# Kernel tuning notes

Hardware: AMD Instinct MI355X
Metric: run time of the kernel (lower is better)

The kernel has to match this reference:

```python
import jax, jax.numpy as jnp
import numpy as np
import math

INPUT_SIZE = 512
DK = 64
B, N = 8, 2048

def setup_inputs() -> dict:
    key = jax.random.key(0)
    k1, k2, k3, k4, k5, k6 = jax.random.split(key, 6)
    X = jax.random.normal(k1, (B, N, INPUT_SIZE), dtype=jnp.float32)
    h = jax.random.normal(k2, (B, N, INPUT_SIZE), dtype=jnp.float32)
    s = 1.0 / math.sqrt(INPUT_SIZE)
    WQ = jax.random.uniform(k3, (INPUT_SIZE, DK), dtype=jnp.float32, minval=-s, maxval=s)
    bQ = jax.random.uniform(k4, (DK,), dtype=jnp.float32, minval=-s, maxval=s)
    WK = jax.random.uniform(k5, (INPUT_SIZE, DK), dtype=jnp.float32, minval=-s, maxval=s)
    bK = jax.random.uniform(k6, (DK,), dtype=jnp.float32, minval=-s, maxval=s)
    return {"X": X, "h": h, "WQ": WQ, "bQ": bQ, "WK": WK, "bK": bK}

def reference(X, h, WQ, bQ, WK, bK):
    # Q = linearQ(h), K = linearK(X); dropout is eval-mode identity
    Q = jnp.einsum('bnd,dk->bnk', h, WQ) + bQ   # [B, N, dk]
    K = jnp.einsum('bnd,dk->bnk', X, WK) + bK   # [B, N, dk]
    scores = jnp.einsum('bqk,bnk->bqn', Q, K) / jnp.sqrt(jnp.asarray(DK, X.dtype))
    A = jax.nn.softmax(scores, axis=-1)          # [B, N, N]
    out = jnp.einsum('bqn,bnd->bqd', A, X)       # V = X
    return out
```

## Files before the change

### kernel.cpp

```cpp
#include <hip/hip_runtime.h>
#include <hip/hip_bf16.h>

#define B_ 8
#define N_ 2048
#define D_ 512
#define DK_ 64

typedef float f32x4 __attribute__((ext_vector_type(4)));
typedef short bf16x8 __attribute__((ext_vector_type(8)));
typedef unsigned short u16;

__device__ __forceinline__ u16 f2bf(float f) {
  union { float f; unsigned u; } v; v.f = f;
  unsigned r = v.u + 0x7FFFu + ((v.u >> 16) & 1u);
  return (u16)(r >> 16);
}

#define MFMA32(a, b, cacc) __builtin_amdgcn_mfma_f32_16x16x32_bf16((a), (b), (cacc), 0, 0, 0)

#define BARRIER_LGKM() do {                                   \
    asm volatile("s_waitcnt lgkmcnt(0)" ::: "memory");        \
    __builtin_amdgcn_s_barrier();                             \
    asm volatile("" ::: "memory");                            \
  } while (0)


__global__ __launch_bounds__(256) void prep_kernel(
    const float* __restrict__ h, const float* __restrict__ X,
    const float* __restrict__ WQ, const float* __restrict__ bQ,
    const float* __restrict__ WK, const float* __restrict__ bK,
    u16* __restrict__ Qf, u16* __restrict__ Kf, u16* __restrict__ Vf) {
  int bid = blockIdx.x;
  int b = bid & 7, nt = bid >> 3;
  int n0 = nt * 64;
  int t = threadIdx.x, w = t >> 6, l = t & 63, g = l >> 4, c = l & 15;

  __shared__ u16 Xb16[64][520];

  int arow = n0 + w * 16 + c;
  const float* hrow = h + ((size_t)b * N_ + arow) * D_;
  const float* Xrow = X + ((size_t)b * N_ + arow) * D_;
  f32x4 accq[4], acck[4];
#pragma unroll
  for (int cf = 0; cf < 4; ++cf) {
    accq[cf] = (f32x4){0.f, 0.f, 0.f, 0.f};
    acck[cf] = (f32x4){0.f, 0.f, 0.f, 0.f};
  }
  for (int k0 = 0; k0 < D_; k0 += 32) {
    bf16x8 ah, ax;
    {
      f32x4 h0 = *reinterpret_cast<const f32x4*>(hrow + k0 + 8 * g);
      f32x4 h1 = *reinterpret_cast<const f32x4*>(hrow + k0 + 8 * g + 4);
      f32x4 x0 = *reinterpret_cast<const f32x4*>(Xrow + k0 + 8 * g);
      f32x4 x1 = *reinterpret_cast<const f32x4*>(Xrow + k0 + 8 * g + 4);
#pragma unroll
      for (int i = 0; i < 4; ++i) {
        ah[i] = (short)f2bf(h0[i]); ah[i + 4] = (short)f2bf(h1[i]);
        ax[i] = (short)f2bf(x0[i]); ax[i + 4] = (short)f2bf(x1[i]);
      }
    }
    *reinterpret_cast<bf16x8*>(&Xb16[w * 16 + c][k0 + 8 * g]) = ax;
#pragma unroll
    for (int cf = 0; cf < 4; ++cf) {
      bf16x8 bq, bk;
#pragma unroll
      for (int i = 0; i < 8; ++i) {
        int kk = k0 + 8 * g + i;
        bq[i] = (short)f2bf(WQ[(size_t)kk * DK_ + cf * 16 + c]);
        bk[i] = (short)f2bf(WK[(size_t)kk * DK_ + cf * 16 + c]);
      }
      accq[cf] = MFMA32(ah, bq, accq[cf]);
      acck[cf] = MFMA32(ax, bk, acck[cf]);
    }
  }

#pragma unroll
  for (int cf = 0; cf < 4; ++cf) {
    float vq = bQ[cf * 16 + c], vk = bK[cf * 16 + c];
    int ks = cf >> 1;
    int g2 = ((cf & 1) * 16 + c) >> 3;
    int i2 = c & 7;
#pragma unroll
    for (int r = 0; r < 4; ++r) {
      size_t e = ((size_t)(b * 128 + nt * 4 + w) * 2 + ks) * 512 +
                 (g2 * 16 + 4 * g + r) * 8 + i2;
      Qf[e] = f2bf((accq[cf][r] + vq) * 0.125f);
      Kf[e] = f2bf(acck[cf][r] + vk);
    }
  }

  __syncthreads();

#pragma unroll
  for (int dtl = 0; dtl < 8; ++dtl) {
    int dt = w * 8 + dtl;
#pragma unroll
    for (int ks = 0; ks < 2; ++ks) {
      bf16x8 v;
#pragma unroll
      for (int i = 0; i < 8; ++i) v[i] = Xb16[ks * 32 + 8 * g + i][dt * 16 + c];
      *reinterpret_cast<bf16x8*>(
          Vf + (((size_t)(b * 32 + dt) * 32 + nt) * 2 + ks) * 512 + l * 8) = v;
    }
  }
}

__global__ __launch_bounds__(512, 1) void attn_kernel(
    const u16* __restrict__ Qf, const u16* __restrict__ Kf,
    const u16* __restrict__ Vf, float* __restrict__ out) {
  int bid = blockIdx.x;
  int b = bid & 7, qt = bid >> 3;
  int q0 = qt * 64;
  int t = threadIdx.x, w = t >> 6, l = t & 63, g = l >> 4, c = l & 15;
  int qh = w >> 1, kq = w & 1;

  __shared__ u16 Plds[2][64][40];
  __shared__ float Lp[2][64];

  bf16x8 aq[2];
#pragma unroll
  for (int ks = 0; ks < 2; ++ks)
    aq[ks] = *reinterpret_cast<const bf16x8*>(
        Qf + ((size_t)(b * 128 + qt * 4 + qh) * 2 + ks) * 512 + l * 8);

  f32x4 o[4][4];
#pragma unroll
  for (int a = 0; a < 4; ++a)
#pragma unroll
    for (int d = 0; d < 4; ++d) o[a][d] = (f32x4){0.f, 0.f, 0.f, 0.f};
  float lp[4] = {0.f, 0.f, 0.f, 0.f};

  const u16* Kbase = Kf + ((size_t)(b * 256 + 2 * kq)) * 512 + l * 8;
  const u16* Vbase = Vf + ((size_t)(b * 32 + w * 4) * 64) * 512 + l * 8;

  bf16x8 kbuf[4][2], vbuf[4][4];

#pragma unroll
  for (int j = 0; j < 3; ++j) {
#pragma unroll
    for (int ks = 0; ks < 2; ++ks)
      kbuf[j][ks] = *reinterpret_cast<const bf16x8*>(
          Kbase + (size_t)(4 * j + ks) * 512);
#pragma unroll
    for (int f = 0; f < 4; ++f)
      vbuf[j][f] = *reinterpret_cast<const bf16x8*>(
          Vbase + (size_t)(f * 64 + j) * 512);
  }
  {
    f32x4 s = (f32x4){0.f, 0.f, 0.f, 0.f};
    s = MFMA32(aq[0], kbuf[0][0], s);
    s = MFMA32(aq[1], kbuf[0][1], s);
#pragma unroll
    for (int r = 0; r < 4; ++r) {
      float p = __expf(s[r]); lp[r] += p;
      Plds[0][qh * 16 + 4 * g + r][kq * 16 + c] = f2bf(p);
    }
  }
  BARRIER_LGKM();

  auto body = [&](bf16x8 (&kS)[2], bf16x8 (&kL)[2],
                  bf16x8 (&vR)[4], bf16x8 (&vL)[4], int i) {
    const int kvL = (i + 3) & 63;
    const int pbW = (i + 1) & 1, pbR = i & 1;

#pragma unroll
    for (int ks = 0; ks < 2; ++ks)
      kL[ks] = *reinterpret_cast<const bf16x8*>(
          Kbase + (size_t)(4 * kvL + ks) * 512);
#pragma unroll
    for (int f = 0; f < 4; ++f)
      vL[f] = *reinterpret_cast<const bf16x8*>(
          Vbase + (size_t)(f * 64 + kvL) * 512);

    f32x4 s = (f32x4){0.f, 0.f, 0.f, 0.f};
    s = MFMA32(aq[0], kS[0], s);
    s = MFMA32(aq[1], kS[1], s);

#pragma unroll
    for (int r = 0; r < 4; ++r) {
      float p = __expf(s[r]); lp[r] += p;
      Plds[pbW][qh * 16 + 4 * g + r][kq * 16 + c] = f2bf(p);
    }

    bf16x8 pa0 = *reinterpret_cast<const bf16x8*>(&Plds[pbR][c][8 * g]);
    bf16x8 pa1 = *reinterpret_cast<const bf16x8*>(&Plds[pbR][16 + c][8 * g]);
    bf16x8 pa2 = *reinterpret_cast<const bf16x8*>(&Plds[pbR][32 + c][8 * g]);
    bf16x8 pa3 = *reinterpret_cast<const bf16x8*>(&Plds[pbR][48 + c][8 * g]);
    __builtin_amdgcn_s_setprio(1);
#pragma unroll
    for (int dt = 0; dt < 4; ++dt) {
      o[0][dt] = MFMA32(pa0, vR[dt], o[0][dt]);
      o[1][dt] = MFMA32(pa1, vR[dt], o[1][dt]);
      o[2][dt] = MFMA32(pa2, vR[dt], o[2][dt]);
      o[3][dt] = MFMA32(pa3, vR[dt], o[3][dt]);
    }
    __builtin_amdgcn_s_setprio(0);

    BARRIER_LGKM();
  };

#pragma unroll 1
  for (int i = 0; i < 60; i += 4) {
    body(kbuf[1], kbuf[3], vbuf[0], vbuf[3], i);
    body(kbuf[2], kbuf[0], vbuf[1], vbuf[0], i + 1);
    body(kbuf[3], kbuf[1], vbuf[2], vbuf[1], i + 2);
    body(kbuf[0], kbuf[2], vbuf[3], vbuf[2], i + 3);
  }
  body(kbuf[1], kbuf[3], vbuf[0], vbuf[3], 60);
  body(kbuf[2], kbuf[0], vbuf[1], vbuf[0], 61);
  body(kbuf[3], kbuf[1], vbuf[2], vbuf[1], 62);

  {
    bf16x8 pa0 = *reinterpret_cast<const bf16x8*>(&Plds[1][c][8 * g]);
    bf16x8 pa1 = *reinterpret_cast<const bf16x8*>(&Plds[1][16 + c][8 * g]);
    bf16x8 pa2 = *reinterpret_cast<const bf16x8*>(&Plds[1][32 + c][8 * g]);
    bf16x8 pa3 = *reinterpret_cast<const bf16x8*>(&Plds[1][48 + c][8 * g]);
#pragma unroll
    for (int dt = 0; dt < 4; ++dt) {
      o[0][dt] = MFMA32(pa0, vbuf[3][dt], o[0][dt]);
      o[1][dt] = MFMA32(pa1, vbuf[3][dt], o[1][dt]);
      o[2][dt] = MFMA32(pa2, vbuf[3][dt], o[2][dt]);
      o[3][dt] = MFMA32(pa3, vbuf[3][dt], o[3][dt]);
    }
  }

#pragma unroll
  for (int r = 0; r < 4; ++r) {
    float v = lp[r];
    v += __shfl_xor(v, 1); v += __shfl_xor(v, 2);
    v += __shfl_xor(v, 4); v += __shfl_xor(v, 8);
    lp[r] = v;
  }
  if (c == 0) {
#pragma unroll
    for (int r = 0; r < 4; ++r) Lp[kq][qh * 16 + 4 * g + r] = lp[r];
  }
  __syncthreads();

  float* outb = out + ((size_t)b * N_ + q0) * D_;
#pragma unroll
  for (int qf2 = 0; qf2 < 4; ++qf2)
#pragma unroll
    for (int r = 0; r < 4; ++r) {
      int ql = qf2 * 16 + 4 * g + r;
      float L = Lp[0][ql] + Lp[1][ql];
      float inv = 1.0f / L;
#pragma unroll
      for (int df = 0; df < 4; ++df)
        outb[(size_t)ql * D_ + w * 64 + df * 16 + c] = o[qf2][df][r] * inv;
    }
}

extern "C" void kernel_launch(void* const* d_in, const int* in_sizes, int n_in,
                              void* d_out, int out_size, void* d_ws, size_t ws_size,
                              hipStream_t stream) {
  const float* X  = (const float*)d_in[0];
  const float* h  = (const float*)d_in[1];
  const float* WQ = (const float*)d_in[2];
  const float* bQ = (const float*)d_in[3];
  const float* WK = (const float*)d_in[4];
  const float* bK = (const float*)d_in[5];
  float* out = (float*)d_out;

  u16* Vf = (u16*)d_ws;
  u16* Qf = Vf + (size_t)B_ * D_ * N_;
  u16* Kf = Qf + (size_t)B_ * N_ * DK_;

  prep_kernel<<<dim3(256), dim3(256), 0, stream>>>(h, X, WQ, bQ, WK, bK, Qf, Kf, Vf);
  attn_kernel<<<dim3(256), dim3(512), 0, stream>>>(Qf, Kf, Vf, out);
}
```

Measured before the change: 76.98 us.

## Process two key tiles per barrier with four-deep P buffers in attention loop

The attention main loop now handles two 32-key tiles per iteration instead of one. It writes two P tiles and consumes two previously written ones from a four-slot LDS ring, so the number of block-wide barriers is halved. V reloads are issued right after each PV MFMA group, reusing that register set, and the prologue and epilogue are rebuilt for the paired schedule. The cost is extra LDS for the P ring and a longer dependency distance whose correctness relies on careful buffer indexing.

New measurement: 73.36 us (median of 2 runs). 4.7% less time.

```diff
diff --git a/kernel.cpp b/kernel.cpp
--- a/kernel.cpp
+++ b/kernel.cpp
@@ -73,7 +73,6 @@
       acck[cf] = MFMA32(ax, bk, acck[cf]);
     }
   }
-
 #pragma unroll
   for (int cf = 0; cf < 4; ++cf) {
     float vq = bQ[cf * 16 + c], vk = bK[cf * 16 + c];
@@ -114,7 +113,7 @@
   int t = threadIdx.x, w = t >> 6, l = t & 63, g = l >> 4, c = l & 15;
   int qh = w >> 1, kq = w & 1;
 
-  __shared__ u16 Plds[2][64][40];
+  __shared__ u16 Plds[4][64][40];
   __shared__ float Lp[2][64];
 
   bf16x8 aq[2];
@@ -136,7 +135,7 @@
   bf16x8 kbuf[4][2], vbuf[4][4];
 
 #pragma unroll
-  for (int j = 0; j < 3; ++j) {
+  for (int j = 0; j < 4; ++j) {
 #pragma unroll
     for (int ks = 0; ks < 2; ++ks)
       kbuf[j][ks] = *reinterpret_cast<const bf16x8*>(
@@ -146,81 +145,118 @@
       vbuf[j][f] = *reinterpret_cast<const bf16x8*>(
           Vbase + (size_t)(f * 64 + j) * 512);
   }
-  {
+#pragma unroll
+  for (int j0 = 0; j0 < 2; ++j0) {
     f32x4 s = (f32x4){0.f, 0.f, 0.f, 0.f};
-    s = MFMA32(aq[0], kbuf[0][0], s);
-    s = MFMA32(aq[1], kbuf[0][1], s);
+    s = MFMA32(aq[0], kbuf[j0][0], s);
+    s = MFMA32(aq[1], kbuf[j0][1], s);
 #pragma unroll
     for (int r = 0; r < 4; ++r) {
       float p = __expf(s[r]); lp[r] += p;
-      Plds[0][qh * 16 + 4 * g + r][kq * 16 + c] = f2bf(p);
+      Plds[j0][qh * 16 + 4 * g + r][kq * 16 + c] = f2bf(p);
     }
   }
   BARRIER_LGKM();
 
-  auto body = [&](bf16x8 (&kS)[2], bf16x8 (&kL)[2],
-                  bf16x8 (&vR)[4], bf16x8 (&vL)[4], int i) {
-    const int kvL = (i + 3) & 63;
-    const int pbW = (i + 1) & 1, pbR = i & 1;
+  auto pair = [&](bf16x8 (&kS0)[2], bf16x8 (&kS1)[2],
+                  bf16x8 (&kL0)[2], bf16x8 (&kL1)[2],
+                  bf16x8 (&vR0)[4], bf16x8 (&vR1)[4],
+                  int k2, int pW0, int pW1, int pR0, int pR1) {
+    const int jA = (k2 + 4) & 63, jB = (k2 + 5) & 63;
 
 #pragma unroll
     for (int ks = 0; ks < 2; ++ks)
-      kL[ks] = *reinterpret_cast<const bf16x8*>(
-          Kbase + (size_t)(4 * kvL + ks) * 512);
+      kL0[ks] = *reinterpret_cast<const bf16x8*>(
+          Kbase + (size_t)(4 * jA + ks) * 512);
+#pragma unroll
+    for (int ks = 0; ks < 2; ++ks)
+      kL1[ks] = *reinterpret_cast<const bf16x8*>(
+          Kbase + (size_t)(4 * jB + ks) * 512);
+
+    {
+      f32x4 s = (f32x4){0.f, 0.f, 0.f, 0.f};
+      s = MFMA32(aq[0], kS0[0], s);
+      s = MFMA32(aq[1], kS0[1], s);
+#pragma unroll
+      for (int r = 0; r < 4; ++r) {
+        float p = __expf(s[r]); lp[r] += p;
+        Plds[pW0][qh * 16 + 4 * g + r][kq * 16 + c] = f2bf(p);
+      }
+    }
+    {
+      f32x4 s = (f32x4){0.f, 0.f, 0.f, 0.f};
+      s = MFMA32(aq[0], kS1[0], s);
+      s = MFMA32(aq[1], kS1[1], s);
+#pragma unroll
+      for (int r = 0; r < 4; ++r) {
+        float p = __expf(s[r]); lp[r] += p;
+        Plds[pW1][qh * 16 + 4 * g + r][kq * 16 + c] = f2bf(p);
+      }
+    }
+
+    {
+      bf16x8 pa0 = *reinterpret_cast<const bf16x8*>(&Plds[pR0][c][8 * g]);
+      bf16x8 pa1 = *reinterpret_cast<const bf16x8*>(&Plds[pR0][16 + c][8 * g]);
+      bf16x8 pa2 = *reinterpret_cast<const bf16x8*>(&Plds[pR0][32 + c][8 * g]);
+      bf16x8 pa3 = *reinterpret_cast<const bf16x8*>(&Plds[pR0][48 + c][8 * g]);
+      __builtin_amdgcn_s_setprio(1);
+#pragma unroll
+      for (int dt = 0; dt < 4; ++dt) {
+        o[0][dt] = MFMA32(pa0, vR0[dt], o[0][dt]);
+        o[1][dt] = MFMA32(pa1, vR0[dt], o[1][dt]);
+        o[2][dt] = MFMA32(pa2, vR0[dt], o[2][dt]);
+        o[3][dt] = MFMA32(pa3, vR0[dt], o[3][dt]);
+      }
+      __builtin_amdgcn_s_setprio(0);
+    }
 #pragma unroll
     for (int f = 0; f < 4; ++f)
-      vL[f] = *reinterpret_cast<const bf16x8*>(
-          Vbase + (size_t)(f * 64 + kvL) * 512);
-
-    f32x4 s = (f32x4){0.f, 0.f, 0.f, 0.f};
-    s = MFMA32(aq[0], kS[0], s);
-    s = MFMA32(aq[1], kS[1], s);
-
-#pragma unroll
-    for (int r = 0; r < 4; ++r) {
-      float p = __expf(s[r]); lp[r] += p;
-      Plds[pbW][qh * 16 + 4 * g + r][kq * 16 + c] = f2bf(p);
-    }
-
-    bf16x8 pa0 = *reinterpret_cast<const bf16x8*>(&Plds[pbR][c][8 * g]);
-    bf16x8 pa1 = *reinterpret_cast<const bf16x8*>(&Plds[pbR][16 + c][8 * g]);
-    bf16x8 pa2 = *reinterpret_cast<const bf16x8*>(&Plds[pbR][32 + c][8 * g]);
-    bf16x8 pa3 = *reinterpret_cast<const bf16x8*>(&Plds[pbR][48 + c][8 * g]);
-    __builtin_amdgcn_s_setprio(1);
-#pragma unroll
-    for (int dt = 0; dt < 4; ++dt) {
-      o[0][dt] = MFMA32(pa0, vR[dt], o[0][dt]);
-      o[1][dt] = MFMA32(pa1, vR[dt], o[1][dt]);
-      o[2][dt] = MFMA32(pa2, vR[dt], o[2][dt]);
-      o[3][dt] = MFMA32(pa3, vR[dt], o[3][dt]);
-    }
-    __builtin_amdgcn_s_setprio(0);
+      vR0[f] = *reinterpret_cast<const bf16x8*>(
+          Vbase + (size_t)(f * 64 + jA) * 512);
+
+    {
+      bf16x8 pa0 = *reinterpret_cast<const bf16x8*>(&Plds[pR1][c][8 * g]);
+      bf16x8 pa1 = *reinterpret_cast<const bf16x8*>(&Plds[pR1][16 + c][8 * g]);
+      bf16x8 pa2 = *reinterpret_cast<const bf16x8*>(&Plds[pR1][32 + c][8 * g]);
+      bf16x8 pa3 = *reinterpret_cast<const bf16x8*>(&Plds[pR1][48 + c][8 * g]);
+      __builtin_amdgcn_s_setprio(1);
+#pragma unroll
+      for (int dt = 0; dt < 4; ++dt) {
+        o[0][dt] = MFMA32(pa0, vR1[dt], o[0][dt]);
+        o[1][dt] = MFMA32(pa1, vR1[dt], o[1][dt]);
+        o[2][dt] = MFMA32(pa2, vR1[dt], o[2][dt]);
+        o[3][dt] = MFMA32(pa3, vR1[dt], o[3][dt]);
+      }
+      __builtin_amdgcn_s_setprio(0);
+    }
+#pragma unroll
+    for (int f = 0; f < 4; ++f)
+      vR1[f] = *reinterpret_cast<const bf16x8*>(
+          Vbase + (size_t)(f * 64 + jB) * 512);
 
     BARRIER_LGKM();
   };
 
 #pragma unroll 1
-  for (int i = 0; i < 60; i += 4) {
-    body(kbuf[1], kbuf[3], vbuf[0], vbuf[3], i);
-    body(kbuf[2], kbuf[0], vbuf[1], vbuf[0], i + 1);
-    body(kbuf[3], kbuf[1], vbuf[2], vbuf[1], i + 2);
-    body(kbuf[0], kbuf[2], vbuf[3], vbuf[2], i + 3);
-  }
-  body(kbuf[1], kbuf[3], vbuf[0], vbuf[3], 60);
-  body(kbuf[2], kbuf[0], vbuf[1], vbuf[0], 61);
-  body(kbuf[3], kbuf[1], vbuf[2], vbuf[1], 62);
-
-  {
-    bf16x8 pa0 = *reinterpret_cast<const bf16x8*>(&Plds[1][c][8 * g]);
-    bf16x8 pa1 = *reinterpret_cast<const bf16x8*>(&Plds[1][16 + c][8 * g]);
-    bf16x8 pa2 = *reinterpret_cast<const bf16x8*>(&Plds[1][32 + c][8 * g]);
-    bf16x8 pa3 = *reinterpret_cast<const bf16x8*>(&Plds[1][48 + c][8 * g]);
+  for (int k2 = 0; k2 < 60; k2 += 4) {
+    pair(kbuf[2], kbuf[3], kbuf[0], kbuf[1], vbuf[0], vbuf[1], k2,     2, 3, 0, 1);
+    pair(kbuf[0], kbuf[1], kbuf[2], kbuf[3], vbuf[2], vbuf[3], k2 + 2, 0, 1, 2, 3);
+  }
+  pair(kbuf[2], kbuf[3], kbuf[0], kbuf[1], vbuf[0], vbuf[1], 60, 2, 3, 0, 1);
+
+#pragma unroll
+  for (int e = 0; e < 2; ++e) {
+    const int pb = 2 + e;
+    bf16x8 pa0 = *reinterpret_cast<const bf16x8*>(&Plds[pb][c][8 * g]);
+    bf16x8 pa1 = *reinterpret_cast<const bf16x8*>(&Plds[pb][16 + c][8 * g]);
+    bf16x8 pa2 = *reinterpret_cast<const bf16x8*>(&Plds[pb][32 + c][8 * g]);
+    bf16x8 pa3 = *reinterpret_cast<const bf16x8*>(&Plds[pb][48 + c][8 * g]);
 #pragma unroll
     for (int dt = 0; dt < 4; ++dt) {
-      o[0][dt] = MFMA32(pa0, vbuf[3][dt], o[0][dt]);
-      o[1][dt] = MFMA32(pa1, vbuf[3][dt], o[1][dt]);
-      o[2][dt] = MFMA32(pa2, vbuf[3][dt], o[2][dt]);
-      o[3][dt] = MFMA32(pa3, vbuf[3][dt], o[3][dt]);
+      o[0][dt] = MFMA32(pa0, vbuf[pb][dt], o[0][dt]);
+      o[1][dt] = MFMA32(pa1, vbuf[pb][dt], o[1][dt]);
+      o[2][dt] = MFMA32(pa2, vbuf[pb][dt], o[2][dt]);
+      o[3][dt] = MFMA32(pa3, vbuf[pb][dt], o[3][dt]);
     }
   }
 
```

## Batch four KV steps per barrier with eight-slot P buffer in attention loop

Applied to the files above, without the earlier changes.

Restructures the attention main loop to process four 32-key steps per group, using an 8-slot LDS P buffer and 8-deep K register prefetch, so a workgroup barrier is issued once per four steps instead of every step. V loads are refilled right after each PV MFMA consumes them. This cuts barrier overhead and gives more independent work between syncs, at the cost of more LDS and more registers, which could cause spills.

After: 76.94 us. No clear change (-0.1%).

```diff
diff --git a/kernel.cpp b/kernel.cpp
--- a/kernel.cpp
+++ b/kernel.cpp
@@ -73,7 +73,6 @@
       acck[cf] = MFMA32(ax, bk, acck[cf]);
     }
   }
-
 #pragma unroll
   for (int cf = 0; cf < 4; ++cf) {
     float vq = bQ[cf * 16 + c], vk = bK[cf * 16 + c];
@@ -114,7 +113,7 @@
   int t = threadIdx.x, w = t >> 6, l = t & 63, g = l >> 4, c = l & 15;
   int qh = w >> 1, kq = w & 1;
 
-  __shared__ u16 Plds[2][64][40];
+  __shared__ u16 Plds[8][64][40];
   __shared__ float Lp[2][64];
 
   bf16x8 aq[2];
@@ -133,94 +132,100 @@
   const u16* Kbase = Kf + ((size_t)(b * 256 + 2 * kq)) * 512 + l * 8;
   const u16* Vbase = Vf + ((size_t)(b * 32 + w * 4) * 64) * 512 + l * 8;
 
-  bf16x8 kbuf[4][2], vbuf[4][4];
-
-#pragma unroll
-  for (int j = 0; j < 3; ++j) {
+  bf16x8 kbuf[8][2], vbuf[4][4];
+
+#pragma unroll
+  for (int j = 0; j < 8; ++j)
 #pragma unroll
     for (int ks = 0; ks < 2; ++ks)
       kbuf[j][ks] = *reinterpret_cast<const bf16x8*>(
           Kbase + (size_t)(4 * j + ks) * 512);
 #pragma unroll
+  for (int j = 0; j < 4; ++j)
+#pragma unroll
     for (int f = 0; f < 4; ++f)
       vbuf[j][f] = *reinterpret_cast<const bf16x8*>(
           Vbase + (size_t)(f * 64 + j) * 512);
-  }
-  {
+#pragma unroll
+  for (int j0 = 0; j0 < 4; ++j0) {
     f32x4 s = (f32x4){0.f, 0.f, 0.f, 0.f};
-    s = MFMA32(aq[0], kbuf[0][0], s);
-    s = MFMA32(aq[1], kbuf[0][1], s);
+    s = MFMA32(aq[0], kbuf[j0][0], s);
+    s = MFMA32(aq[1], kbuf[j0][1], s);
 #pragma unroll
     for (int r = 0; r < 4; ++r) {
       float p = __expf(s[r]); lp[r] += p;
-      Plds[0][qh * 16 + 4 * g + r][kq * 16 + c] = f2bf(p);
+      Plds[j0][qh * 16 + 4 * g + r][kq * 16 + c] = f2bf(p);
     }
   }
   BARRIER_LGKM();
 
-  auto body = [&](bf16x8 (&kS)[2], bf16x8 (&kL)[2],
-                  bf16x8 (&vR)[4], bf16x8 (&vL)[4], int i) {
-    const int kvL = (i + 3) & 63;
-    const int pbW = (i + 1) & 1, pbR = i & 1;
-
-#pragma unroll
-    for (int ks = 0; ks < 2; ++ks)
-      kL[ks] = *reinterpret_cast<const bf16x8*>(
-          Kbase + (size_t)(4 * kvL + ks) * 512);
-#pragma unroll
-    for (int f = 0; f < 4; ++f)
-      vL[f] = *reinterpret_cast<const bf16x8*>(
-          Vbase + (size_t)(f * 64 + kvL) * 512);
-
-    f32x4 s = (f32x4){0.f, 0.f, 0.f, 0.f};
-    s = MFMA32(aq[0], kS[0], s);
-    s = MFMA32(aq[1], kS[1], s);
-
-#pragma unroll
-    for (int r = 0; r < 4; ++r) {
-      float p = __expf(s[r]); lp[r] += p;
-      Plds[pbW][qh * 16 + 4 * g + r][kq * 16 + c] = f2bf(p);
-    }
-
-    bf16x8 pa0 = *reinterpret_cast<const bf16x8*>(&Plds[pbR][c][8 * g]);
-    bf16x8 pa1 = *reinterpret_cast<const bf16x8*>(&Plds[pbR][16 + c][8 * g]);
-    bf16x8 pa2 = *reinterpret_cast<const bf16x8*>(&Plds[pbR][32 + c][8 * g]);
-    bf16x8 pa3 = *reinterpret_cast<const bf16x8*>(&Plds[pbR][48 + c][8 * g]);
-    __builtin_amdgcn_s_setprio(1);
-#pragma unroll
-    for (int dt = 0; dt < 4; ++dt) {
-      o[0][dt] = MFMA32(pa0, vR[dt], o[0][dt]);
-      o[1][dt] = MFMA32(pa1, vR[dt], o[1][dt]);
-      o[2][dt] = MFMA32(pa2, vR[dt], o[2][dt]);
-      o[3][dt] = MFMA32(pa3, vR[dt], o[3][dt]);
-    }
-    __builtin_amdgcn_s_setprio(0);
+  auto group = [&](int k4, int sB, int lB) {
+#pragma unroll
+    for (int j = 0; j < 4; ++j) {
+      const int jk = (k4 + 8 + j) & 63;
+#pragma unroll
+      for (int ks = 0; ks < 2; ++ks)
+        kbuf[lB + j][ks] = *reinterpret_cast<const bf16x8*>(
+            Kbase + (size_t)(4 * jk + ks) * 512);
+    }
+
+#pragma unroll
+    for (int j = 0; j < 4; ++j) {
+      f32x4 s = (f32x4){0.f, 0.f, 0.f, 0.f};
+      s = MFMA32(aq[0], kbuf[sB + j][0], s);
+      s = MFMA32(aq[1], kbuf[sB + j][1], s);
+#pragma unroll
+      for (int r = 0; r < 4; ++r) {
+        float p = __expf(s[r]); lp[r] += p;
+        Plds[sB + j][qh * 16 + 4 * g + r][kq * 16 + c] = f2bf(p);
+      }
+    }
+
+#pragma unroll
+    for (int j = 0; j < 4; ++j) {
+      bf16x8 pa0 = *reinterpret_cast<const bf16x8*>(&Plds[lB + j][c][8 * g]);
+      bf16x8 pa1 = *reinterpret_cast<const bf16x8*>(&Plds[lB + j][16 + c][8 * g]);
+      bf16x8 pa2 = *reinterpret_cast<const bf16x8*>(&Plds[lB + j][32 + c][8 * g]);
+      bf16x8 pa3 = *reinterpret_cast<const bf16x8*>(&Plds[lB + j][48 + c][8 * g]);
+      __builtin_amdgcn_s_setprio(1);
+#pragma unroll
+      for (int dt = 0; dt < 4; ++dt) {
+        o[0][dt] = MFMA32(pa0, vbuf[j][dt], o[0][dt]);
+        o[1][dt] = MFMA32(pa1, vbuf[j][dt], o[1][dt]);
+        o[2][dt] = MFMA32(pa2, vbuf[j][dt], o[2][dt]);
+        o[3][dt] = MFMA32(pa3, vbuf[j][dt], o[3][dt]);
+      }
+      __builtin_amdgcn_s_setprio(0);
+      const int jv = (k4 + 4 + j) & 63;
+#pragma unroll
+      for (int f = 0; f < 4; ++f)
+        vbuf[j][f] = *reinterpret_cast<const bf16x8*>(
+            Vbase + (size_t)(f * 64 + jv) * 512);
+    }
 
     BARRIER_LGKM();
   };
 
 #pragma unroll 1
-  for (int i = 0; i < 60; i += 4) {
-    body(kbuf[1], kbuf[3], vbuf[0], vbuf[3], i);
-    body(kbuf[2], kbuf[0], vbuf[1], vbuf[0], i + 1);
-    body(kbuf[3], kbuf[1], vbuf[2], vbuf[1], i + 2);
-    body(kbuf[0], kbuf[2], vbuf[3], vbuf[2], i + 3);
-  }
-  body(kbuf[1], kbuf[3], vbuf[0], vbuf[3], 60);
-  body(kbuf[2], kbuf[0], vbuf[1], vbuf[0], 61);
-  body(kbuf[3], kbuf[1], vbuf[2], vbuf[1], 62);
-
-  {
-    bf16x8 pa0 = *reinterpret_cast<const bf16x8*>(&Plds[1][c][8 * g]);
-    bf16x8 pa1 = *reinterpret_cast<const bf16x8*>(&Plds[1][16 + c][8 * g]);
-    bf16x8 pa2 = *reinterpret_cast<const bf16x8*>(&Plds[1][32 + c][8 * g]);
-    bf16x8 pa3 = *reinterpret_cast<const bf16x8*>(&Plds[1][48 + c][8 * g]);
+  for (int k4 = 0; k4 < 56; k4 += 8) {
+    group(k4, 4, 0);
+    group(k4 + 4, 0, 4);
+  }
+  group(56, 4, 0);
+
+#pragma unroll
+  for (int j = 0; j < 4; ++j) {
+    const int pb = 4 + j;
+    bf16x8 pa0 = *reinterpret_cast<const bf16x8*>(&Plds[pb][c][8 * g]);
+    bf16x8 pa1 = *reinterpret_cast<const bf16x8*>(&Plds[pb][16 + c][8 * g]);
+    bf16x8 pa2 = *reinterpret_cast<const bf16x8*>(&Plds[pb][32 + c][8 * g]);
+    bf16x8 pa3 = *reinterpret_cast<const bf16x8*>(&Plds[pb][48 + c][8 * g]);
 #pragma unroll
     for (int dt = 0; dt < 4; ++dt) {
-      o[0][dt] = MFMA32(pa0, vbuf[3][dt], o[0][dt]);
-      o[1][dt] = MFMA32(pa1, vbuf[3][dt], o[1][dt]);
-      o[2][dt] = MFMA32(pa2, vbuf[3][dt], o[2][dt]);
-      o[3][dt] = MFMA32(pa3, vbuf[3][dt], o[3][dt]);
+      o[0][dt] = MFMA32(pa0, vbuf[j][dt], o[0][dt]);
+      o[1][dt] = MFMA32(pa1, vbuf[j][dt], o[1][dt]);
+      o[2][dt] = MFMA32(pa2, vbuf[j][dt], o[2][dt]);
+      o[3][dt] = MFMA32(pa3, vbuf[j][dt], o[3][dt]);
     }
   }
 
```
